# Kernel optimization log

Hardware: AMD Instinct MI355X
Metric: run time of the kernel (lower is better)

Reference implementation:

```python
import jax, jax.numpy as jnp
import numpy as np

N, E = 20000, 320000
IN_CH, HID, NPRED = 64, 512, 12
NUM_GCN = 3   # num_gcn_layers=4 -> 1 + (4-2) layers
NUM_RNN = 2
BN_EPS = 1e-5


def setup_inputs() -> dict:
    key = jax.random.key(0)
    ks = jax.random.split(key, 16)
    s = 0.05  # init scale to keep activations sane
    return {
        "x": jax.random.normal(ks[0], (N, IN_CH), jnp.float32),
        "edge_index": jax.random.randint(ks[1], (2, E), 0, N, jnp.int32),
        "edge_weight": jax.random.uniform(ks[2], (E,), jnp.float32),
        "gcn0_W": jax.random.normal(ks[3], (IN_CH, HID), jnp.float32) * s,
        "gcn0_b": jnp.zeros((HID,), jnp.float32),
        "gcn_W": jax.random.normal(ks[4], (NUM_GCN - 1, HID, HID), jnp.float32) * s,
        "gcn_b": jnp.zeros((NUM_GCN - 1, HID), jnp.float32),
        "bn_gamma": jnp.ones((NUM_GCN, HID), jnp.float32),
        "bn_beta": jnp.zeros((NUM_GCN, HID), jnp.float32),
        "w_ih": jax.random.normal(ks[5], (NUM_RNN, HID, 4 * HID), jnp.float32) * s,
        "w_hh": jax.random.normal(ks[6], (NUM_RNN, HID, 4 * HID), jnp.float32) * s,
        "w_ch": jax.random.normal(ks[7], (NUM_RNN, HID, 3 * HID), jnp.float32) * s,
        "lstm_b": jnp.zeros((NUM_RNN, 4 * HID), jnp.float32),
        "out_W": jax.random.normal(ks[8], (HID, NPRED), jnp.float32) * s,
        "out_b": jnp.zeros((NPRED,), jnp.float32),
    }


def _gcn(x, W, b, src, dst, ew, n):
    h = x @ W                                   # [N, out]
    msg = ew[:, None] * h[src]                  # [E, out]
    return jax.ops.segment_sum(msg, dst, num_segments=n) + b


def _bn_relu(x, gamma, beta):
    mu = jnp.mean(x, axis=0)
    var = jnp.var(x, axis=0)
    return jax.nn.relu((x - mu) * jax.lax.rsqrt(var + BN_EPS) * gamma + beta)


def _peephole_cell(inp, h, c, Wih, Whh, Wch, b):
    H = h.shape[1]
    gates = inp @ Wih + h @ Whh + b             # [N, 4H]
    i_g, f_g, g_g, o_g = jnp.split(gates, 4, axis=1)
    g_g = g_g + c @ Wch[:, :H]
    i_g = jax.nn.sigmoid(i_g)
    f_g = jax.nn.sigmoid(f_g + c @ Wch[:, H:2 * H])
    g_g = jnp.tanh(g_g)
    cy = f_g * c + i_g * g_g
    o_g = o_g + cy @ Wch[:, 2 * H:]
    hy = jax.nn.sigmoid(o_g) * jnp.tanh(cy)
    return hy, cy


def reference(x, edge_index, edge_weight, gcn0_W, gcn0_b, gcn_W, gcn_b,
              bn_gamma, bn_beta, w_ih, w_hh, w_ch, lstm_b, out_W, out_b):
    src, dst = edge_index[0], edge_index[1]
    n = x.shape[0]
    # GCN stack: conv -> batchnorm (train-mode stats) -> relu (dropout=0)
    h = _gcn(x, gcn0_W, gcn0_b, src, dst, edge_weight, n)
    h = _bn_relu(h, bn_gamma[0], bn_beta[0])
    for i in range(NUM_GCN - 1):
        h = _gcn(h, gcn_W[i], gcn_b[i], src, dst, edge_weight, n)
        h = _bn_relu(h, bn_gamma[i + 1], bn_beta[i + 1])
    # seq_len == 1 after unsqueeze; cells chained sharing (h_t, c_t)
    h_t = jnp.zeros((n, HID), h.dtype)
    c_t = jnp.zeros((n, HID), h.dtype)
    for l in range(NUM_RNN):
        h_t, c_t = _peephole_cell(h, h_t, c_t, w_ih[l], w_hh[l], w_ch[l], lstm_b[l])
    out = h_t @ out_W + out_b                   # [N, num_predictions]
    return jnp.squeeze(out)
```

## Files before the change

### kernel.cpp

```cpp
#include <hip/hip_runtime.h>
#include <cstddef>

#define N_NODES 20000
#define N_EDGES 320000
#define IN_CH   64
#define HID     512
#define G4      2048
#define BN_EPS  1e-5f
#define F_OFF   0
#define G_OFF   512
#define I_OFF   1024
#define O_OFF   1536

typedef __attribute__((ext_vector_type(8))) __bf16 bf16x8;
typedef __attribute__((ext_vector_type(4))) float f32x4;

__device__ __forceinline__ float sigmoidf_(float x) {
  return 1.0f / (1.0f + expf(-x));
}

__device__ __forceinline__ unsigned short f2b(float f) {
  unsigned int u = __float_as_uint(f);
  u += 0x7FFFu + ((u >> 16) & 1u);
  return (unsigned short)(u >> 16);
}
__device__ __forceinline__ float b2f(unsigned short u) {
  return __uint_as_float(((unsigned int)u) << 16);
}

__device__ __forceinline__ void gld_lds16(const unsigned short* g, unsigned short* l) {
  __builtin_amdgcn_global_load_lds(
      (const __attribute__((address_space(1))) unsigned int*)(const void*)g,
      (__attribute__((address_space(3))) unsigned int*)(void*)l, 16, 0, 0);
}

__global__ __launch_bounds__(256) void zero_k(float* __restrict__ p, size_t n) {
  size_t i = ((size_t)blockIdx.x * 256 + threadIdx.x) * 4;
  if (i + 3 < n) {
    *(float4*)&p[i] = make_float4(0.f, 0.f, 0.f, 0.f);
  } else {
    for (; i < n; i++) p[i] = 0.f;
  }
}

__global__ __launch_bounds__(256) void cvt_k(const float* __restrict__ in,
                                             unsigned short* __restrict__ out, size_t n) {
  size_t i = ((size_t)blockIdx.x * 256 + threadIdx.x) * 4;
  if (i + 3 < n) {
    const float4 v = *(const float4*)&in[i];
    ushort4 o; o.x = f2b(v.x); o.y = f2b(v.y); o.z = f2b(v.z); o.w = f2b(v.w);
    *(ushort4*)&out[i] = o;
  } else {
    for (; i < n; i++) out[i] = f2b(in[i]);
  }
}

struct TcvtDesc { const float* W; unsigned short* Wt; int K, NC, ldw, ldo; };
struct TcvtBatch { TcvtDesc d[18]; };

__global__ void tcvtb_k(TcvtBatch batch) {
  const TcvtDesc dd = batch.d[blockIdx.z];
  __shared__ float tile[32][33];
  const int n0 = blockIdx.x * 32, k0 = blockIdx.y * 32;
  if (n0 >= dd.NC || k0 >= dd.K) return;
  const int tx = threadIdx.x, ty = threadIdx.y;
  #pragma unroll
  for (int i = 0; i < 32; i += 8) {
    int k = k0 + ty + i, n = n0 + tx;
    tile[ty + i][tx] = (k < dd.K && n < dd.NC) ? dd.W[(size_t)k * dd.ldw + n] : 0.f;
  }
  __syncthreads();
  #pragma unroll
  for (int i = 0; i < 32; i += 8) {
    int n = n0 + ty + i, k = k0 + tx;
    if (n < dd.NC && k < dd.K) dd.Wt[(size_t)n * dd.ldo + k] = f2b(tile[tx][ty + i]);
  }
}

__global__ __launch_bounds__(256) void hist_k(const int* __restrict__ dst,
                                              int* __restrict__ counts) {
  int e = blockIdx.x * 256 + threadIdx.x;
  if (e < N_EDGES) atomicAdd(&counts[dst[e]], 1);
}

__global__ __launch_bounds__(1024) void scan_k(const int* __restrict__ counts,
                                               int* __restrict__ offsets,
                                               int* __restrict__ pos, int n) {
  __shared__ int tmp[1024];
  __shared__ int carry_s;
  const int tid = threadIdx.x;
  if (tid == 0) carry_s = 0;
  __syncthreads();
  for (int base = 0; base < n; base += 1024) {
    int i = base + tid;
    int v = (i < n) ? counts[i] : 0;
    tmp[tid] = v;
    __syncthreads();
    #pragma unroll
    for (int off = 1; off < 1024; off <<= 1) {
      int t = (tid >= off) ? tmp[tid - off] : 0;
      __syncthreads();
      tmp[tid] += t;
      __syncthreads();
    }
    if (i < n) {
      int excl = carry_s + tmp[tid] - v;
      offsets[i] = excl;
      pos[i] = excl;
    }
    __syncthreads();
    if (tid == 1023) carry_s += tmp[1023];
    __syncthreads();
  }
  if (tid == 0) offsets[n] = carry_s;
}

__global__ __launch_bounds__(256) void fill_k(
    const int* __restrict__ src, const int* __restrict__ dst,
    const float* __restrict__ ew, int* __restrict__ pos,
    int* __restrict__ s_s, float* __restrict__ w_s) {
  int e = blockIdx.x * 256 + threadIdx.x;
  if (e >= N_EDGES) return;
  int p = atomicAdd(&pos[dst[e]], 1);
  s_s[p] = src[e];
  w_s[p] = ew[e];
}

__global__ __launch_bounds__(64) void gather64_k(
    const unsigned short* __restrict__ x16, const int* __restrict__ offsets,
    const int* __restrict__ s_s, const float* __restrict__ w_s,
    unsigned short* __restrict__ xg) {
  const int sub = threadIdx.x >> 4;
  const int cg  = threadIdx.x & 15;
  const int n   = blockIdx.x * 4 + sub;
  const int beg = offsets[n], end = offsets[n + 1];
  float4 acc = make_float4(0.f, 0.f, 0.f, 0.f);
  for (int i = beg; i < end; i++) {
    const int   s = s_s[i];
    const float w = w_s[i];
    const ushort4 v = *(const ushort4*)&x16[(size_t)s * IN_CH + cg * 4];
    acc.x = fmaf(w, b2f(v.x), acc.x);
    acc.y = fmaf(w, b2f(v.y), acc.y);
    acc.z = fmaf(w, b2f(v.z), acc.z);
    acc.w = fmaf(w, b2f(v.w), acc.w);
  }
  ushort4 o; o.x = f2b(acc.x); o.y = f2b(acc.y); o.z = f2b(acc.z); o.w = f2b(acc.w);
  *(ushort4*)&xg[(size_t)n * IN_CH + cg * 4] = o;
}

__global__ __launch_bounds__(128) void gather_k(
    const unsigned short* __restrict__ XW, const int* __restrict__ offsets,
    const int* __restrict__ s_s, const float* __restrict__ w_s,
    unsigned short* __restrict__ H) {
  const int n = blockIdx.x;
  const int t = threadIdx.x;
  const int beg = offsets[n], end = offsets[n + 1];
  float4 acc = make_float4(0.f, 0.f, 0.f, 0.f);
  for (int i = beg; i < end; i++) {
    const int   s = s_s[i];
    const float w = w_s[i];
    const ushort4 v = *(const ushort4*)&XW[(size_t)s * HID + t * 4];
    acc.x = fmaf(w, b2f(v.x), acc.x);
    acc.y = fmaf(w, b2f(v.y), acc.y);
    acc.z = fmaf(w, b2f(v.z), acc.z);
    acc.w = fmaf(w, b2f(v.w), acc.w);
  }
  ushort4 o; o.x = f2b(acc.x); o.y = f2b(acc.y); o.z = f2b(acc.z); o.w = f2b(acc.w);
  *(ushort4*)&H[(size_t)n * HID + t * 4] = o;
}

__global__ __launch_bounds__(256) void bn_stats_k(
    const unsigned short* __restrict__ H, float* __restrict__ stats, int N)
{
  const int tx = threadIdx.x & 63;
  const int ty = threadIdx.x >> 6;
  const int col = blockIdx.x * 64 + tx;
  float s1 = 0.f, s2 = 0.f;
  for (int r = blockIdx.y * 4 + ty; r < N; r += gridDim.y * 4) {
    float v = b2f(H[(size_t)r * HID + col]);
    s1 += v; s2 += v * v;
  }
  __shared__ float red[2][4][64];
  red[0][ty][tx] = s1;
  red[1][ty][tx] = s2;
  __syncthreads();
  if (ty == 0) {
    s1 = red[0][0][tx] + red[0][1][tx] + red[0][2][tx] + red[0][3][tx];
    s2 = red[1][0][tx] + red[1][1][tx] + red[1][2][tx] + red[1][3][tx];
    atomicAdd(&stats[col], s1);
    atomicAdd(&stats[HID + col], s2);
  }
}

__global__ __launch_bounds__(256) void bn_apply_k(
    const unsigned short* __restrict__ H, const float* __restrict__ stats,
    const float* __restrict__ gamma, const float* __restrict__ beta,
    unsigned short* __restrict__ out, int N)
{
  size_t gid = (size_t)blockIdx.x * 256 + threadIdx.x;
  size_t idx = gid * 4;
  if (idx >= (size_t)N * HID) return;
  int col = (int)(idx & (HID - 1));
  const ushort4 v = *(const ushort4*)&H[idx];
  float r[4] = {b2f(v.x), b2f(v.y), b2f(v.z), b2f(v.w)};
  ushort4 o;
  unsigned short* op = &o.x;
  #pragma unroll
  for (int i = 0; i < 4; i++) {
    int c = col + i;
    float mean = stats[c] * (1.0f / N);
    float var  = stats[HID + c] * (1.0f / N) - mean * mean;
    float scale = gamma[c] / sqrtf(var + BN_EPS);
    float shift = beta[c] - mean * scale;
    op[i] = f2b(fmaxf(fmaf(r[i], scale, shift), 0.0f));
  }
  *(ushort4*)&out[idx] = o;
}

template<int BM, int BN>
__global__ __launch_bounds__(256) void gemm_bf16_k(
    const unsigned short* __restrict__ A, int lda,
    const unsigned short* __restrict__ A2, int lda2, int ksplit,
    const unsigned short* __restrict__ Bt,
    float* __restrict__ C, unsigned short* __restrict__ C16,
    const float* __restrict__ bias,
    int M, int K, int Ksmall, int NC, int ldc, int acc, int nrowb, int ncolb)
{
  const int b   = blockIdx.x;
  const int xcd = b & 7;
  const int j   = b >> 3;
  const int col_b = j % ncolb;
  const int row_b = (j / ncolb) * 8 + xcd;
  if (row_b >= nrowb) return;

  constexpr int MI  = 2;
  constexpr int ASZ = BM * 64;
  constexpr int BSZ = BN * 64;
  __shared__ unsigned short As[2 * ASZ];
  __shared__ unsigned short Bs[2 * BSZ];
  const int row0 = row_b * BM;
  const int col0 = col_b * BN;
  const int Kthis = (col0 < 1024) ? K : Ksmall;
  const int t    = threadIdx.x;
  const int lane = t & 63;
  const int w    = t >> 6;
  const int wro  = (BN == 128) ? (w >> 1) * 32 : w * 32;
  const int wco  = (BN == 128) ? (w & 1) * 64 : 0;
  const int q    = lane >> 4;
  const int l16  = lane & 15;

  f32x4 accr[MI][4] = {};

  auto stage = [&](int buf, int k0) {
    unsigned short* Ad = As + buf * ASZ;
    unsigned short* Bd = Bs + buf * BSZ;
    #pragma unroll
    for (int i = 0; i < BM / 32; i++) {
      int s  = t + i * 256;
      int r  = s >> 3, cq = s & 7;
      int kq = (cq - r) & 7;
      int gr = row0 + r; if (gr > M - 1) gr = M - 1;
      int kk = k0 + kq * 8;
      const unsigned short* bp = (kk < ksplit) ? A : A2;
      size_t off = (kk < ksplit) ? ((size_t)gr * lda + kk)
                                 : ((size_t)gr * lda2 + (kk - ksplit));
      gld_lds16(bp + off, Ad + (size_t)s * 8);
    }
    #pragma unroll
    for (int i = 0; i < BN / 32; i++) {
      int s  = t + i * 256;
      int r  = s >> 3, cq = s & 7;
      int kq = (cq - r) & 7;
      gld_lds16(Bt + (size_t)(col0 + r) * K + k0 + kq * 8, Bd + (size_t)s * 8);
    }
  };

  stage(0, 0);
  int cur = 0;
  for (int k0 = 0; k0 < Kthis; k0 += 64) {
    __syncthreads();
    if (k0 + 64 < Kthis) stage(cur ^ 1, k0 + 64);

    const unsigned short* Ac = As + cur * ASZ;
    const unsigned short* Bc = Bs + cur * BSZ;
    #pragma unroll
    for (int ks = 0; ks < 2; ks++) {
      bf16x8 af[MI], bfr[4];
      #pragma unroll
      for (int mi = 0; mi < MI; mi++) {
        int r = wro + mi * 16 + l16;
        int slot = (ks * 4 + q + r) & 7;
        af[mi] = *(const bf16x8*)&Ac[r * 64 + slot * 8];
      }
      #pragma unroll
      for (int ni = 0; ni < 4; ni++) {
        int r = wco + ni * 16 + l16;
        int slot = (ks * 4 + q + r) & 7;
        bfr[ni] = *(const bf16x8*)&Bc[r * 64 + slot * 8];
      }
      #pragma unroll
      for (int mi = 0; mi < MI; mi++)
        #pragma unroll
        for (int ni = 0; ni < 4; ni++)
          accr[mi][ni] = __builtin_amdgcn_mfma_f32_16x16x32_bf16(
              af[mi], bfr[ni], accr[mi][ni], 0, 0, 0);
    }
    cur ^= 1;
  }

  #pragma unroll
  for (int mi = 0; mi < MI; mi++) {
    #pragma unroll
    for (int ni = 0; ni < 4; ni++) {
      int col = col0 + wco + ni * 16 + l16;
      #pragma unroll
      for (int r = 0; r < 4; r++) {
        int row = row0 + wro + mi * 16 + q * 4 + r;
        if (row < M) {
          float v = accr[mi][ni][r];
          if (C16) {
            C16[(size_t)row * ldc + col] = f2b(v);
          } else {
            float* cp = &C[(size_t)row * ldc + col];
            if (acc)       *cp += v;
            else if (bias) *cp  = v + bias[col];
            else           *cp  = v;
          }
        }
      }
    }
  }
}

__global__ __launch_bounds__(256) void cell1_k(
    const float* __restrict__ gates, const float* __restrict__ lb,
    const float* __restrict__ cin,
    float* __restrict__ cout, unsigned short* __restrict__ cout16, int ld16,
    int rows, int hasC)
{
  size_t gid = (size_t)blockIdx.x * 256 + threadIdx.x;
  if (gid >= (size_t)rows * HID) return;
  size_t row = gid >> 9;
  int    col = (int)(gid & (HID - 1));
  const float* g = &gates[row * G4];
  float ig = sigmoidf_(g[I_OFF + col] + lb[col]);
  float gg = tanhf(g[G_OFF + col] + lb[2 * HID + col]);
  float c;
  if (hasC) {
    float fg = sigmoidf_(g[F_OFF + col] + lb[HID + col]);
    c = fg * cin[gid] + ig * gg;
  } else {
    c = ig * gg;
  }
  cout[gid] = c;
  cout16[row * ld16 + col] = f2b(c);
}

__global__ __launch_bounds__(256) void cell2_k(
    const float* __restrict__ gates, const float* __restrict__ obuf,
    const float* __restrict__ lb, const float* __restrict__ cy,
    unsigned short* __restrict__ hy16, int ld16, int rows)
{
  size_t gid = (size_t)blockIdx.x * 256 + threadIdx.x;
  if (gid >= (size_t)rows * HID) return;
  size_t row = gid >> 9;
  int    col = (int)(gid & (HID - 1));
  float og = sigmoidf_(gates[row * G4 + O_OFF + col] + obuf[gid] + lb[3 * HID + col]);
  float h = og * tanhf(cy[gid]);
  hy16[row * ld16 + col] = f2b(h);
}

__global__ __launch_bounds__(256) void cellout_k(
    const float* __restrict__ gates, const float* __restrict__ obuf,
    const float* __restrict__ lb, const float* __restrict__ cy,
    const float* __restrict__ W, const float* __restrict__ b,
    float* __restrict__ out, int rows)
{
  int wave = (int)(((size_t)blockIdx.x * 256 + threadIdx.x) >> 6);
  int lane = threadIdx.x & 63;
  if (wave >= rows) return;
  const float* g  = &gates[(size_t)wave * G4 + O_OFF];
  const float* ob = &obuf[(size_t)wave * HID];
  const float* cr = &cy[(size_t)wave * HID];
  float hy[8];
  #pragma unroll
  for (int j = 0; j < 8; j++) {
    int k = lane + j * 64;
    float og = sigmoidf_(g[k] + ob[k] + lb[3 * HID + k]);
    hy[j] = og * tanhf(cr[k]);
  }
  float acc[12] = {};
  #pragma unroll
  for (int j = 0; j < 8; j++) {
    int k = lane + j * 64;
    const float* wr = &W[k * 12];
    #pragma unroll
    for (int p = 0; p < 12; p++) acc[p] = fmaf(hy[j], wr[p], acc[p]);
  }
  #pragma unroll
  for (int p = 0; p < 12; p++) {
    float v = acc[p];
    #pragma unroll
    for (int off = 32; off > 0; off >>= 1) v += __shfl_down(v, off);
    if (lane == 0) out[(size_t)wave * 12 + p] = v + b[p];
  }
}

extern "C" void kernel_launch(void* const* d_in, const int* in_sizes, int n_in,
                              void* d_out, int out_size, void* d_ws, size_t ws_size,
                              hipStream_t stream) {
  const float* x     = (const float*)d_in[0];
  const int*   ei    = (const int*)d_in[1];
  const float* ew    = (const float*)d_in[2];
  const float* gcn0W = (const float*)d_in[3];
  const float* gcnW  = (const float*)d_in[5];
  const float* gamma = (const float*)d_in[7];
  const float* beta  = (const float*)d_in[8];
  const float* wih   = (const float*)d_in[9];
  const float* whh   = (const float*)d_in[10];
  const float* wch   = (const float*)d_in[11];
  const float* lstmb = (const float*)d_in[12];
  const float* outW  = (const float*)d_in[13];
  const float* outb  = (const float*)d_in[14];
  float* out = (float*)d_out;

  const int* src = ei;
  const int* dst = ei + N_EDGES;

  const int CH = (ws_size >= (size_t)215000000) ? 10000 : 5000;
  const int NCHUNK = N_NODES / CH;

  const size_t NH = (size_t)N_NODES * HID;
  float* ws = (float*)d_ws;
  float* gates = ws;
  float* bufH  = gates + (size_t)CH * G4;
  unsigned short* hbA16 = (unsigned short*)(bufH + NH);
  unsigned short* hbB16 = hbA16 + NH;
  unsigned short* x16   = hbB16 + NH;
  unsigned short* g0t   = x16 + (size_t)N_NODES * IN_CH;
  unsigned short* g1t   = g0t   + 512 * 64;
  unsigned short* g2t   = g1t   + 512 * 512;
  unsigned short* wih0t = g2t   + 512 * 512;
  unsigned short* wcat3 = wih0t + (size_t)1536 * 512;
  unsigned short* wch0ot= wcat3 + (size_t)2048 * 1536;
  unsigned short* wch1ot= wch0ot + 512 * 512;
  unsigned short* wend  = wch1ot + 512 * 512;
  unsigned short *a16, *tail16;
  if (CH == 5000) {
    a16  = hbB16;
    tail16 = wend;
  } else {
    a16  = wend;
    tail16 = a16 + (size_t)CH * 1024;
  }
  float* stats = (float*)tail16;
  int*   csr   = (int*)(stats + 3072);
  int*   counts  = csr;
  int*   offsets = csr + 20032;
  int*   cpos    = csr + 40064;
  int*   s_s     = csr + 60096;
  float* w_s     = (float*)(csr + 380096);

  unsigned short* bufH16 = (unsigned short*)bufH;
  float* cbuf = bufH;
  float* obuf = bufH + (size_t)CH * HID;

  const dim3 blk(256);
  auto gemm128 = [&](const unsigned short* A, int lda,
                     const unsigned short* A2, int lda2, int ksplit,
                     const unsigned short* Bt, float* C, unsigned short* C16,
                     const float* bias, int M, int K, int Ksmall, int NC, int ldc,
                     int acc) {
    int nrowb = (M + 63) / 64;
    int ncolb = NC / 128;
    int nblocks = 8 * ((nrowb + 7) / 8) * ncolb;
    hipLaunchKernelGGL((gemm_bf16_k<64, 128>), dim3(nblocks), blk, 0, stream,
                       A, lda, A2, lda2, ksplit, Bt, C, C16, bias,
                       M, K, Ksmall, NC, ldc, acc, nrowb, ncolb);
  };
  auto gemm64 = [&](const unsigned short* A, int lda,
                    const unsigned short* Bt, float* C, unsigned short* C16,
                    const float* bias, int M, int K, int NC, int ldc, int acc) {
    int nrowb = (M + 127) / 128;
    int ncolb = NC / 64;
    int nblocks = 8 * ((nrowb + 7) / 8) * ncolb;
    hipLaunchKernelGGL((gemm_bf16_k<128, 64>), dim3(nblocks), blk, 0, stream,
                       A, lda, A, lda, K, Bt, C, C16, bias,
                       M, K, K, NC, ldc, acc, nrowb, ncolb);
  };
  auto zero = [&](float* p, size_t n) {
    hipLaunchKernelGGL(zero_k, dim3((unsigned)((n / 4 + 255) / 256)), blk, 0, stream, p, n);
  };

  const float* wih1 = wih + (size_t)HID * G4;
  const float* whh1 = whh + (size_t)HID * G4;
  const float* wch1 = wch + (size_t)HID * 3 * HID;
  {
    TcvtBatch tb;
    int n = 0;
    auto add = [&](const float* W, unsigned short* Wt, int K, int NC, int ldw, int ldo) {
      tb.d[n++] = TcvtDesc{W, Wt, K, NC, ldw, ldo};
    };
    add(gcn0W, g0t, IN_CH, HID, HID, IN_CH);
    add(gcnW,                     g1t, HID, HID, HID, HID);
    add(gcnW + (size_t)HID * HID, g2t, HID, HID, HID, HID);
    add(wih + 2 * HID, wih0t,                      HID, HID, G4, HID);
    add(wih,           wih0t + (size_t)512 * 512,  HID, HID, G4, HID);
    add(wih + 3 * HID, wih0t + (size_t)1024 * 512, HID, HID, G4, HID);
    add(wih1 + HID,     wcat3 + (size_t)F_OFF * 1536,        HID, HID, G4, 1536);
    add(whh1 + HID,     wcat3 + (size_t)F_OFF * 1536 + 512,  HID, HID, G4, 1536);
    add(wch1 + HID,     wcat3 + (size_t)F_OFF * 1536 + 1024, HID, HID, 3 * HID, 1536);
    add(wih1 + 2 * HID, wcat3 + (size_t)G_OFF * 1536,        HID, HID, G4, 1536);
    add(whh1 + 2 * HID, wcat3 + (size_t)G_OFF * 1536 + 512,  HID, HID, G4, 1536);
    add(wch1,           wcat3 + (size_t)G_OFF * 1536 + 1024, HID, HID, 3 * HID, 1536);
    add(wih1,           wcat3 + (size_t)I_OFF * 1536,        HID, HID, G4, 1536);
    add(whh1,           wcat3 + (size_t)I_OFF * 1536 + 512,  HID, HID, G4, 1536);
    add(wih1 + 3 * HID, wcat3 + (size_t)O_OFF * 1536,        HID, HID, G4, 1536);
    add(whh1 + 3 * HID, wcat3 + (size_t)O_OFF * 1536 + 512,  HID, HID, G4, 1536);
    add(wch + 2 * HID,  wch0ot, HID, HID, 3 * HID, HID);
    add(wch1 + 2 * HID, wch1ot, HID, HID, 3 * HID, HID);
    hipLaunchKernelGGL(tcvtb_k, dim3(16, 16, 18), dim3(32, 8), 0, stream, tb);
  }
  hipLaunchKernelGGL(cvt_k, dim3((N_NODES * IN_CH / 4 + 255) / 256), blk, 0, stream,
                     x, x16, (size_t)N_NODES * IN_CH);

  const int e_blocks = (N_EDGES + 255) / 256;
  zero((float*)counts, N_NODES);
  zero(stats, 3 * 1024);
  hipLaunchKernelGGL(hist_k, dim3(e_blocks), blk, 0, stream, dst, counts);
  hipLaunchKernelGGL(scan_k, dim3(1), dim3(1024), 0, stream, counts, offsets, cpos, N_NODES);
  hipLaunchKernelGGL(fill_k, dim3(e_blocks), blk, 0, stream, src, dst, ew, cpos, s_s, w_s);

  hipLaunchKernelGGL(gather64_k, dim3(N_NODES / 4), dim3(64), 0, stream,
                     x16, offsets, s_s, w_s, hbB16);
  gemm64(hbB16, IN_CH, g0t, nullptr, bufH16, nullptr, N_NODES, IN_CH, HID, HID, 0);
  hipLaunchKernelGGL(bn_stats_k, dim3(8, 64), blk, 0, stream, bufH16, stats, N_NODES);
  hipLaunchKernelGGL(bn_apply_k, dim3((unsigned)(NH / 4 / 256)), blk, 0, stream,
                     bufH16, stats, gamma, beta, hbA16, N_NODES);

  const unsigned short* gWt2[2] = {g1t, g2t};
  const unsigned short* gA2[2]  = {hbA16, hbB16};
  unsigned short*       gXW2[2] = {hbB16, hbA16};
  unsigned short*       gO2[2]  = {hbB16, hbA16};
  for (int l = 0; l < 2; l++) {
    gemm64(gA2[l], HID, gWt2[l], nullptr, gXW2[l], nullptr, N_NODES, HID, HID, HID, 0);
    hipLaunchKernelGGL(gather_k, dim3(N_NODES), dim3(128), 0, stream,
                       gXW2[l], offsets, s_s, w_s, bufH16);
    hipLaunchKernelGGL(bn_stats_k, dim3(8, 64), blk, 0, stream, bufH16,
                       stats + (l + 1) * 1024, N_NODES);
    hipLaunchKernelGGL(bn_apply_k, dim3((unsigned)(NH / 4 / 256)), blk, 0, stream,
                       bufH16, stats + (l + 1) * 1024, gamma + (l + 1) * HID,
                       beta + (l + 1) * HID, gO2[l], N_NODES);
  }
  unsigned short* hfin16 = hbA16;

  for (int ci = 0; ci < NCHUNK; ci++) {
    const int r0 = ci * CH;
    const unsigned short* h_c = hfin16 + (size_t)r0 * HID;
    const int cell_blocks = (int)(((size_t)CH * HID + 255) / 256);

    gemm128(h_c, HID, h_c, HID, HID, wih0t, gates + G_OFF, nullptr, nullptr,
            CH, HID, HID, 1536, G4, 0);
    hipLaunchKernelGGL(cell1_k, dim3(cell_blocks), blk, 0, stream,
                       gates, lstmb, (const float*)nullptr, cbuf, a16 + 512, 1024, CH, 0);
    gemm64(a16 + 512, 1024, wch0ot, obuf, nullptr, nullptr, CH, HID, HID, HID, 0);
    hipLaunchKernelGGL(cell2_k, dim3(cell_blocks), blk, 0, stream,
                       gates, obuf, lstmb, cbuf, a16, 1024, CH);

    gemm128(h_c, HID, a16, 1024, HID, wcat3, gates, nullptr, nullptr,
            CH, 1536, 1024, G4, G4, 0);
    hipLaunchKernelGGL(cell1_k, dim3(cell_blocks), blk, 0, stream,
                       gates, lstmb + G4, cbuf, cbuf, a16 + 512, 1024, CH, 1);
    gemm64(a16 + 512, 1024, wch1ot, obuf, nullptr, nullptr, CH, HID, HID, HID, 0);
    hipLaunchKernelGGL(cellout_k, dim3((CH * 64 + 255) / 256), blk, 0, stream,
                       gates, obuf, lstmb + G4, cbuf, outW, outb,
                       out + (size_t)r0 * 12, CH);
  }
}
```

Measured before the change: 887.7 us.

## Fuse LSTM gate GEMM with cell update via gate-interleaved weight layout

After: 892.9 us. No clear change (+0.6%).

```diff
diff --git a/kernel.cpp b/kernel.cpp
--- a/kernel.cpp
+++ b/kernel.cpp
@@ -7,10 +7,6 @@
 #define HID     512
 #define G4      2048
 #define BN_EPS  1e-5f
-#define F_OFF   0
-#define G_OFF   512
-#define I_OFF   1024
-#define O_OFF   1536
 
 typedef __attribute__((ext_vector_type(8))) __bf16 bf16x8;
 typedef __attribute__((ext_vector_type(4))) float f32x4;
@@ -55,8 +51,8 @@
   }
 }
 
-struct TcvtDesc { const float* W; unsigned short* Wt; int K, NC, ldw, ldo; };
-struct TcvtBatch { TcvtDesc d[18]; };
+struct TcvtDesc { const float* W; unsigned short* Wt; int K, NC, ldw, ldo, gate; };
+struct TcvtBatch { TcvtDesc d[19]; };
 
 __global__ void tcvtb_k(TcvtBatch batch) {
   const TcvtDesc dd = batch.d[blockIdx.z];
@@ -73,7 +69,12 @@
   #pragma unroll
   for (int i = 0; i < 32; i += 8) {
     int n = n0 + ty + i, k = k0 + tx;
-    if (n < dd.NC && k < dd.K) dd.Wt[(size_t)n * dd.ldo + k] = f2b(tile[tx][ty + i]);
+    if (n < dd.NC && k < dd.K) {
+      size_t orow = (dd.gate < 0)
+          ? (size_t)n
+          : (size_t)((n >> 4) * 64 + dd.gate * 16 + (n & 15));
+      dd.Wt[orow * dd.ldo + k] = f2b(tile[tx][ty + i]);
+    }
   }
 }
 
@@ -332,32 +333,138 @@
   }
 }
 
-__global__ __launch_bounds__(256) void cell1_k(
-    const float* __restrict__ gates, const float* __restrict__ lb,
-    const float* __restrict__ cin,
-    float* __restrict__ cout, unsigned short* __restrict__ cout16, int ld16,
-    int rows, int hasC)
+__global__ __launch_bounds__(256) void gemm_gates_k(
+    const unsigned short* __restrict__ A, int lda,
+    const unsigned short* __restrict__ A2, int lda2, int ksplit,
+    const unsigned short* __restrict__ Bt,
+    const float* __restrict__ lb, const float* __restrict__ cin,
+    float* __restrict__ cbuf, unsigned short* __restrict__ c16, int ldc16,
+    float* __restrict__ ogat,
+    int M, int K, int Ksmall, int nrowb)
 {
-  size_t gid = (size_t)blockIdx.x * 256 + threadIdx.x;
-  if (gid >= (size_t)rows * HID) return;
-  size_t row = gid >> 9;
-  int    col = (int)(gid & (HID - 1));
-  const float* g = &gates[row * G4];
-  float ig = sigmoidf_(g[I_OFF + col] + lb[col]);
-  float gg = tanhf(g[G_OFF + col] + lb[2 * HID + col]);
-  float c;
-  if (hasC) {
-    float fg = sigmoidf_(g[F_OFF + col] + lb[HID + col]);
-    c = fg * cin[gid] + ig * gg;
-  } else {
-    c = ig * gg;
-  }
-  cout[gid] = c;
-  cout16[row * ld16 + col] = f2b(c);
+  const int b   = blockIdx.x;
+  const int xcd = b & 7;
+  const int j   = b >> 3;
+  const int col_b = j & 15;
+  const int row_b = (j >> 4) * 8 + xcd;
+  if (row_b >= nrowb) return;
+
+  constexpr int ASZ = 64 * 64;
+  constexpr int BSZ = 128 * 64;
+  __shared__ unsigned short As[2 * ASZ];
+  __shared__ unsigned short Bs[2 * BSZ];
+  const int row0 = row_b * 64;
+  const int col0 = col_b * 128;
+  const int t    = threadIdx.x;
+  const int lane = t & 63;
+  const int w    = t >> 6;
+  const int wro  = (w >> 1) * 32;
+  const int wco  = (w & 1) * 64;
+  const int q    = lane >> 4;
+  const int l16  = lane & 15;
+
+  f32x4 accr[2][4] = {};
+
+  auto stage = [&](int buf, int k0) {
+    unsigned short* Ad = As + buf * ASZ;
+    unsigned short* Bd = Bs + buf * BSZ;
+    #pragma unroll
+    for (int i = 0; i < 2; i++) {
+      int s  = t + i * 256;
+      int r  = s >> 3, cq = s & 7;
+      int kq = (cq - r) & 7;
+      int gr = row0 + r; if (gr > M - 1) gr = M - 1;
+      int kk = k0 + kq * 8;
+      const unsigned short* bp = (kk < ksplit) ? A : A2;
+      size_t off = (kk < ksplit) ? ((size_t)gr * lda + kk)
+                                 : ((size_t)gr * lda2 + (kk - ksplit));
+      gld_lds16(bp + off, Ad + (size_t)s * 8);
+    }
+    #pragma unroll
+    for (int i = 0; i < 4; i++) {
+      int s  = t + i * 256;
+      int r  = s >> 3, cq = s & 7;
+      int kq = (cq - r) & 7;
+      gld_lds16(Bt + (size_t)(col0 + r) * K + k0 + kq * 8, Bd + (size_t)s * 8);
+    }
+  };
+
+  stage(0, 0);
+  int cur = 0;
+  for (int k0 = 0; k0 < K; k0 += 64) {
+    __syncthreads();
+    if (k0 + 64 < K) stage(cur ^ 1, k0 + 64);
+
+    const unsigned short* Ac = As + cur * ASZ;
+    const unsigned short* Bc = Bs + cur * BSZ;
+    const bool full = (k0 < Ksmall);
+    #pragma unroll
+    for (int ks = 0; ks < 2; ks++) {
+      bf16x8 af[2];
+      #pragma unroll
+      for (int mi = 0; mi < 2; mi++) {
+        int r = wro + mi * 16 + l16;
+        int slot = (ks * 4 + q + r) & 7;
+        af[mi] = *(const bf16x8*)&Ac[r * 64 + slot * 8];
+      }
+      bf16x8 bfr[4];
+      #pragma unroll
+      for (int ni = 0; ni < 2; ni++) {
+        int r = wco + ni * 16 + l16;
+        int slot = (ks * 4 + q + r) & 7;
+        bfr[ni] = *(const bf16x8*)&Bc[r * 64 + slot * 8];
+      }
+      #pragma unroll
+      for (int mi = 0; mi < 2; mi++)
+        #pragma unroll
+        for (int ni = 0; ni < 2; ni++)
+          accr[mi][ni] = __builtin_amdgcn_mfma_f32_16x16x32_bf16(
+              af[mi], bfr[ni], accr[mi][ni], 0, 0, 0);
+      if (full) {
+        #pragma unroll
+        for (int ni = 2; ni < 4; ni++) {
+          int r = wco + ni * 16 + l16;
+          int slot = (ks * 4 + q + r) & 7;
+          bfr[ni] = *(const bf16x8*)&Bc[r * 64 + slot * 8];
+        }
+        #pragma unroll
+        for (int mi = 0; mi < 2; mi++)
+          #pragma unroll
+          for (int ni = 2; ni < 4; ni++)
+            accr[mi][ni] = __builtin_amdgcn_mfma_f32_16x16x32_bf16(
+                af[mi], bfr[ni], accr[mi][ni], 0, 0, 0);
+      }
+    }
+    cur ^= 1;
+  }
+
+  const int hgrp = (col0 + wco) >> 6;
+  const int h    = hgrp * 16 + l16;
+  const float bi  = lb[h];
+  const float bfv = lb[HID + h];
+  const float bg  = lb[2 * HID + h];
+  #pragma unroll
+  for (int mi = 0; mi < 2; mi++) {
+    #pragma unroll
+    for (int r = 0; r < 4; r++) {
+      int row = row0 + wro + mi * 16 + q * 4 + r;
+      if (row < M) {
+        float fv = accr[mi][0][r], gv = accr[mi][1][r];
+        float iv = accr[mi][2][r], ov = accr[mi][3][r];
+        float ig = sigmoidf_(iv + bi);
+        float gg = tanhf(gv + bg);
+        float c  = cin ? sigmoidf_(fv + bfv) * cin[(size_t)row * HID + h] + ig * gg
+                       : ig * gg;
+        cbuf[(size_t)row * HID + h] = c;
+        c16[(size_t)row * ldc16 + h] = f2b(c);
+        ogat[(size_t)row * HID + h] = ov;
+      }
+    }
+  }
 }
 
 __global__ __launch_bounds__(256) void cell2_k(
-    const float* __restrict__ gates, const float* __restrict__ obuf,
+    const float* __restrict__ ogat, const float* __restrict__ obuf,
     const float* __restrict__ lb, const float* __restrict__ cy,
     unsigned short* __restrict__ hy16, int ld16, int rows)
 {
@@ -365,13 +472,13 @@
   if (gid >= (size_t)rows * HID) return;
   size_t row = gid >> 9;
   int    col = (int)(gid & (HID - 1));
-  float og = sigmoidf_(gates[row * G4 + O_OFF + col] + obuf[gid] + lb[3 * HID + col]);
+  float og = sigmoidf_(ogat[gid] + obuf[gid] + lb[3 * HID + col]);
   float h = og * tanhf(cy[gid]);
   hy16[row * ld16 + col] = f2b(h);
 }
 
 __global__ __launch_bounds__(256) void cellout_k(
-    const float* __restrict__ gates, const float* __restrict__ obuf,
+    const float* __restrict__ ogat, const float* __restrict__ obuf,
     const float* __restrict__ lb, const float* __restrict__ cy,
     const float* __restrict__ W, const float* __restrict__ b,
     float* __restrict__ out, int rows)
@@ -379,7 +486,7 @@
   int wave = (int)(((size_t)blockIdx.x * 256 + threadIdx.x) >> 6);
   int lane = threadIdx.x & 63;
   if (wave >= rows) return;
-  const float* g  = &gates[(size_t)wave * G4 + O_OFF];
+  const float* g  = &ogat[(size_t)wave * HID];
   const float* ob = &obuf[(size_t)wave * HID];
   const float* cr = &cy[(size_t)wave * HID];
   float hy[8];
@@ -441,17 +548,19 @@
   unsigned short* g1t   = g0t   + 512 * 64;
   unsigned short* g2t   = g1t   + 512 * 512;
   unsigned short* wih0t = g2t   + 512 * 512;
-  unsigned short* wcat3 = wih0t + (size_t)1536 * 512;
+  unsigned short* wcat3 = wih0t + (size_t)2048 * 512;
   unsigned short* wch0ot= wcat3 + (size_t)2048 * 1536;
   unsigned short* wch1ot= wch0ot + 512 * 512;
   unsigned short* wend  = wch1ot + 512 * 512;
-  unsigned short *a16, *tail16;
+  unsigned short *a16, *c16o, *tail16;
   if (CH == 5000) {
     a16  = hbB16;
+    c16o = a16 + (size_t)CH * 1024;
     tail16 = wend;
   } else {
     a16  = wend;
-    tail16 = a16 + (size_t)CH * 1024;
+    c16o = a16 + (size_t)CH * 1024;
+    tail16 = c16o + (size_t)CH * 512;
   }
   float* stats = (float*)tail16;
   int*   csr   = (int*)(stats + 3072);
@@ -464,19 +573,19 @@
   unsigned short* bufH16 = (unsigned short*)bufH;
   float* cbuf = bufH;
   float* obuf = bufH + (size_t)CH * HID;
+  float* ogat = gates;
 
   const dim3 blk(256);
-  auto gemm128 = [&](const unsigned short* A, int lda,
-                     const unsigned short* A2, int lda2, int ksplit,
-                     const unsigned short* Bt, float* C, unsigned short* C16,
-                     const float* bias, int M, int K, int Ksmall, int NC, int ldc,
-                     int acc) {
+  auto gemm_gates = [&](const unsigned short* A, int lda,
+                        const unsigned short* A2, int lda2, int ksplit,
+                        const unsigned short* Bt, const float* lb,
+                        const float* cin, float* cb, unsigned short* c16,
+                        int ldc16, int M, int K, int Ksmall) {
     int nrowb = (M + 63) / 64;
-    int ncolb = NC / 128;
-    int nblocks = 8 * ((nrowb + 7) / 8) * ncolb;
-    hipLaunchKernelGGL((gemm_bf16_k<64, 128>), dim3(nblocks), blk, 0, stream,
-                       A, lda, A2, lda2, ksplit, Bt, C, C16, bias,
-                       M, K, Ksmall, NC, ldc, acc, nrowb, ncolb);
+    int nblocks = 8 * ((nrowb + 7) / 8) * 16;
+    hipLaunchKernelGGL(gemm_gates_k, dim3(nblocks), blk, 0, stream,
+                       A, lda, A2, lda2, ksplit, Bt, lb, cin, cb, c16, ldc16,
+                       ogat, M, K, Ksmall, nrowb);
   };
   auto gemm64 = [&](const unsigned short* A, int lda,
                     const unsigned short* Bt, float* C, unsigned short* C16,
@@ -498,28 +607,30 @@
   {
     TcvtBatch tb;
     int n = 0;
-    auto add = [&](const float* W, unsigned short* Wt, int K, int NC, int ldw, int ldo) {
-      tb.d[n++] = TcvtDesc{W, Wt, K, NC, ldw, ldo};
+    auto add = [&](const float* W, unsigned short* Wt, int K, int NC, int ldw,
+                   int ldo, int gate) {
+      tb.d[n++] = TcvtDesc{W, Wt, K, NC, ldw, ldo, gate};
     };
-    add(gcn0W, g0t, IN_CH, HID, HID, IN_CH);
-    add(gcnW,                     g1t, HID, HID, HID, HID);
-    add(gcnW + (size_t)HID * HID, g2t, HID, HID, HID, HID);
-    add(wih + 2 * HID, wih0t,                      HID, HID, G4, HID);
-    add(wih,           wih0t + (size_t)512 * 512,  HID, HID, G4, HID);
-    add(wih + 3 * HID, wih0t + (size_t)1024 * 512, HID, HID, G4, HID);
-    add(wih1 + HID,     wcat3 + (size_t)F_OFF * 1536,        HID, HID, G4, 1536);
-    add(whh1 + HID,     wcat3 + (size_t)F_OFF * 1536 + 512,  HID, HID, G4, 1536);
-    add(wch1 + HID,     wcat3 + (size_t)F_OFF * 1536 + 1024, HID, HID, 3 * HID, 1536);
-    add(wih1 + 2 * HID, wcat3 + (size_t)G_OFF * 1536,        HID, HID, G4, 1536);
-    add(whh1 + 2 * HID, wcat3 + (size_t)G_OFF * 1536 + 512,  HID, HID, G4, 1536);
-    add(wch1,           wcat3 + (size_t)G_OFF * 1536 + 1024, HID, HID, 3 * HID, 1536);
-    add(wih1,           wcat3 + (size_t)I_OFF * 1536,        HID, HID, G4, 1536);
-    add(whh1,           wcat3 + (size_t)I_OFF * 1536 + 512,  HID, HID, G4, 1536);
-    add(wih1 + 3 * HID, wcat3 + (size_t)O_OFF * 1536,        HID, HID, G4, 1536);
-    add(whh1 + 3 * HID, wcat3 + (size_t)O_OFF * 1536 + 512,  HID, HID, G4, 1536);
-    add(wch + 2 * HID,  wch0ot, HID, HID, 3 * HID, HID);
-    add(wch1 + 2 * HID, wch1ot, HID, HID, 3 * HID, HID);
-    hipLaunchKernelGGL(tcvtb_k, dim3(16, 16, 18), dim3(32, 8), 0, stream, tb);
+    add(gcn0W, g0t, IN_CH, HID, HID, IN_CH, -1);
+    add(gcnW,                     g1t, HID, HID, HID, HID, -1);
+    add(gcnW + (size_t)HID * HID, g2t, HID, HID, HID, HID, -1);
+    add(wih + HID,     wih0t, HID, HID, G4, HID, 0);
+    add(wih + 2 * HID, wih0t, HID, HID, G4, HID, 1);
+    add(wih,           wih0t, HID, HID, G4, HID, 2);
+    add(wih + 3 * HID, wih0t, HID, HID, G4, HID, 3);
+    add(wih1 + HID,     wcat3,        HID, HID, G4,      1536, 0);
+    add(whh1 + HID,     wcat3 + 512,  HID, HID, G4,      1536, 0);
+    add(wch1 + HID,     wcat3 + 1024, HID, HID, 3 * HID, 1536, 0);
+    add(wih1 + 2 * HID, wcat3,        HID, HID, G4,      1536, 1);
+    add(whh1 + 2 * HID, wcat3 + 512,  HID, HID, G4,      1536, 1);
+    add(wch1,           wcat3 + 1024, HID, HID, 3 * HID, 1536, 1);
+    add(wih1,           wcat3,        HID, HID, G4,      1536, 2);
+    add(whh1,           wcat3 + 512,  HID, HID, G4,      1536, 2);
+    add(wih1 + 3 * HID, wcat3,        HID, HID, G4,      1536, 3);
+    add(whh1 + 3 * HID, wcat3 + 512,  HID, HID, G4,      1536, 3);
+    add(wch + 2 * HID,  wch0ot, HID, HID, 3 * HID, HID, -1);
+    add(wch1 + 2 * HID, wch1ot, HID, HID, 3 * HID, HID, -1);
+    hipLaunchKernelGGL(tcvtb_k, dim3(16, 16, 19), dim3(32, 8), 0, stream, tb);
   }
   hipLaunchKernelGGL(cvt_k, dim3((N_NODES * IN_CH / 4 + 255) / 256), blk, 0, stream,
                      x, x16, (size_t)N_NODES * IN_CH);
@@ -559,21 +670,17 @@
     const unsigned short* h_c = hfin16 + (size_t)r0 * HID;
     const int cell_blocks = (int)(((size_t)CH * HID + 255) / 256);
 
-    gemm128(h_c, HID, h_c, HID, HID, wih0t, gates + G_OFF, nullptr, nullptr,
-            CH, HID, HID, 1536, G4, 0);
-    hipLaunchKernelGGL(cell1_k, dim3(cell_blocks), blk, 0, stream,
-                       gates, lstmb, (const float*)nullptr, cbuf, a16 + 512, 1024, CH, 0);
+    gemm_gates(h_c, HID, h_c, HID, HID, wih0t, lstmb, nullptr,
+               cbuf, a16 + 512, 1024, CH, HID, HID);
     gemm64(a16 + 512, 1024, wch0ot, obuf, nullptr, nullptr, CH, HID, HID, HID, 0);
     hipLaunchKernelGGL(cell2_k, dim3(cell_blocks), blk, 0, stream,
-                       gates, obuf, lstmb, cbuf, a16, 1024, CH);
-
-    gemm128(h_c, HID, a16, 1024, HID, wcat3, gates, nullptr, nullptr,
-            CH, 1536, 1024, G4, G4, 0);
-    hipLaunchKernelGGL(cell1_k, dim3(cell_blocks), blk, 0, stream,
-                       gates, lstmb + G4, cbuf, cbuf, a16 + 512, 1024, CH, 1);
-    gemm64(a16 + 512, 1024, wch1ot, obuf, nullptr, nullptr, CH, HID, HID, HID, 0);
+                       ogat, obuf, lstmb, cbuf, a16, 1024, CH);
+
+    gemm_gates(h_c, HID, a16, 1024, HID, wcat3, lstmb + G4, cbuf,
+               cbuf, c16o, 512, CH, 3 * HID, 1024);
+    gemm64(c16o, 512, wch1ot, obuf, nullptr, nullptr, CH, HID, HID, HID, 0);
     hipLaunchKernelGGL(cellout_k, dim3((CH * 64 + 255) / 256), blk, 0, stream,
-                       gates, obuf, lstmb + G4, cbuf, outW, outb,
+                       ogat, obuf, lstmb + G4, cbuf, outW, outb,
                        out + (size_t)r0 * 12, CH);
   }
 }
```
